# Performance work log

Hardware: AMD Instinct MI355X
Metric: run time of the kernel (lower is better)

Reference implementation:

```python
import jax, jax.numpy as jnp
import numpy as np

BETA_F = 1000.0
BETA_B = 1.0
CLAMP = 12.0
B, C, H, W = 4, 1, 1024, 1024
N_NODES = 262144  # nodes per max-tree


def soft_mask(logits):
    # forward sigmoid with beta_f gain and +-12 clamp (clamp_logits=True)
    return jax.nn.sigmoid(jnp.clip(BETA_F * logits, -CLAMP, CLAMP))


def tree_filter(sigma, levels, parent):
    """Differentiable connected filtering on one max-tree.
    Node value = level(root) + sum over root->node path of sigma_j*(level_j - level_parent_j),
    computed with pointer-doubling ancestor sums (log N gather passes).
    sigma, levels: (N,), parent: (N,) int32 with parent[0]==0 (root).
    """
    N = sigma.shape[0]
    delta = levels - levels[parent]          # per-node gray-level increment
    c = (sigma * delta).at[0].set(levels[0])  # root contributes its level
    # sentinel node N with contribution 0 and self-pointer, terminates chains
    acc = jnp.concatenate([c, jnp.zeros((1,), c.dtype)])
    ptr = jnp.concatenate([parent.at[0].set(N), jnp.full((1,), N, parent.dtype)])
    steps = int(np.ceil(np.log2(N))) + 1
    for _ in range(steps):
        acc, ptr = acc + acc[ptr], ptr[ptr]
    return acc[:N]


def setup_inputs() -> dict:
    rng = np.random.default_rng(0)
    T = B * C  # one tree per (b, c) image
    idx = np.arange(N_NODES)
    # topologically ordered random tree: parent[i] in [0, i), parent[0] = 0
    parent = np.floor(rng.random((T, N_NODES)) * idx).astype(np.int32)
    # monotone increasing gray levels: ancestor-sum of positive increments
    inc = (rng.random((T, N_NODES)) + 0.1).astype(np.float32)
    acc = np.concatenate([inc, np.zeros((T, 1), np.float32)], 1)
    ptr = np.concatenate([parent, np.full((T, 1), N_NODES, np.int64)], 1)
    ptr[:, 0] = N_NODES
    for _ in range(int(np.ceil(np.log2(N_NODES))) + 1):
        acc = acc + np.take_along_axis(acc, ptr, 1)
        ptr = np.take_along_axis(ptr, ptr, 1)
    levels = acc[:, :N_NODES]
    attr_norm = rng.random((T, N_NODES)).astype(np.float32)  # minmax01-normalized attribute
    pixel_to_node = rng.integers(0, N_NODES, (T, H * W)).astype(np.int32)
    x = rng.standard_normal((B, C, H, W)).astype(np.float32)
    return {
        "x": jnp.asarray(x),
        "attr_norm": jnp.asarray(attr_norm),
        "levels": jnp.asarray(levels),
        "thr": jnp.full((1,), 0.5, jnp.float32),  # torch init.constant_(p, 0.5)
        "parent": jnp.asarray(parent),
        "pixel_to_node": jnp.asarray(pixel_to_node),
    }


def reference(x, attr_norm, levels, thr, parent, pixel_to_node):
    # logits = attr_scaled - threshold_norm, per node, per tree
    sigma = soft_mask(attr_norm - thr.reshape(()))          # (T, N)
    v = jax.vmap(tree_filter)(sigma, levels, parent)         # (T, N) filtered node values
    y = jnp.take_along_axis(v, pixel_to_node, axis=1)        # node -> pixel gather
    return y.reshape(B, C, H, W)  # top_hat=False, num_groups=1 -> out_channels=C
```

## Files before the change

### kernel.cpp

```cpp
#include <hip/hip_runtime.h>

#define NT 4
#define NN 262144
#define NMASK (NN - 1)
#define HW 1048576
#define KPRE 16384

#define SWIZ(b, tree, chunk)                \
    int tree  = ((b) & 7) >> 1;             \
    int chunk = (((b) >> 3) << 1) | ((b) & 1);

__global__ __launch_bounds__(256) void k_build(const float* __restrict__ attr,
                                               const float* __restrict__ levels,
                                               const float* __restrict__ thr,
                                               const int* __restrict__ parent,
                                               int2* __restrict__ cmb) {
    SWIZ(blockIdx.x, tree, chunk)
    int n = chunk * 256 + threadIdx.x;
    int i = (tree << 18) + n;
    int p = parent[i] & NMASK;
    float lv = levels[i];
    float lp = levels[(tree << 18) | p];
    float z = 1000.0f * (attr[i] - thr[0]);
    z = fminf(fmaxf(z, -12.0f), 12.0f);
    float s = 1.0f / (1.0f + __expf(-z));
    float c = s * (lv - lp);
    if (n == 0) { c = lv; p = 0; }
    cmb[i] = make_int2(p, __float_as_int(c));
}

__global__ __launch_bounds__(256) void k_prefix(const int2* __restrict__ cmb,
                                                float* __restrict__ v) {
    SWIZ(blockIdx.x, tree, chunk)
    int node = chunk * 256 + threadIdx.x;
    const int2* ctree = cmb + (tree << 18);
    float acc = 0.0f;
    int cur = node;
    bool alive = true;
    for (int it = 0; it < 64 && __any(alive); ++it) {
        if (alive) {
            int2 rec = ctree[cur];
            acc += __int_as_float(rec.y);
            if (cur == 0) alive = false;
            else cur = rec.x;
        }
    }
    v[(tree << 18) + node] = acc;
}

__global__ __launch_bounds__(256) void k_walk(const int2* __restrict__ cmb,
                                              float* __restrict__ v) {
    SWIZ(blockIdx.x, tree, chunk)
    int base = KPRE + chunk * 1024;
    const int2*  ctree = cmb + (tree << 18);
    const float* vtree = v + (tree << 18);

    int   cur[4];
    float acc[4];
    int alive = 0xF;
#pragma unroll
    for (int k = 0; k < 4; ++k) {
        cur[k] = base + threadIdx.x + k * 256;
        acc[k] = 0.0f;
    }
    for (int it = 0; it < 64 && __any(alive); ++it) {
#pragma unroll
        for (int k = 0; k < 4; ++k) {
            if (alive & (1 << k)) {
                int2 rec = ctree[cur[k]];
                acc[k] += __int_as_float(rec.y);
                int nxt = rec.x;
                if (nxt < KPRE) {
                    acc[k] += vtree[nxt];
                    alive &= ~(1 << k);
                } else {
                    cur[k] = nxt;
                }
            }
        }
    }
#pragma unroll
    for (int k = 0; k < 4; ++k)
        v[(tree << 18) + base + threadIdx.x + k * 256] = acc[k];
}

__global__ __launch_bounds__(256) void k_pix(const float* __restrict__ v,
                                             const int* __restrict__ p2n,
                                             float* __restrict__ y) {
    SWIZ(blockIdx.x, tree, chunk)
    int i = (tree << 18) + chunk * 256 + threadIdx.x;
    int4 idx = ((const int4*)p2n)[i];
    const float* vt = v + (tree << 18);
    float4 o;
    o.x = vt[idx.x & NMASK];
    o.y = vt[idx.y & NMASK];
    o.z = vt[idx.z & NMASK];
    o.w = vt[idx.w & NMASK];
    ((float4*)y)[i] = o;
}

extern "C" void kernel_launch(void* const* d_in, const int* in_sizes, int n_in,
                              void* d_out, int out_size, void* d_ws, size_t ws_size,
                              hipStream_t stream) {
    const float* attr   = (const float*)d_in[1];
    const float* levels = (const float*)d_in[2];
    const float* thr    = (const float*)d_in[3];
    const int*   parent = (const int*)d_in[4];
    const int*   p2n    = (const int*)d_in[5];
    float*       y      = (float*)d_out;

    int2*  cmb = (int2*)d_ws;
    float* v   = (float*)((char*)d_ws + (size_t)NT * NN * sizeof(int2));

    k_build <<<NT * NN / 256, 256, 0, stream>>>(attr, levels, thr, parent, cmb);
    k_prefix<<<NT * KPRE / 256, 256, 0, stream>>>(cmb, v);
    k_walk  <<<NT * (NN - KPRE) / 1024, 256, 0, stream>>>(cmb, v);
    k_pix   <<<NT * HW / 4 / 256, 256, 0, stream>>>(v, p2n, y);
}
```

Baseline: 135.1 us.

## Rebalance two-phase tree walk split point and vectorize build with nontemporal loads

Moves the boundary between the direct root-walk phase and the shortcut phase from 16K to 64K nodes, and makes the second phase walk one node per thread instead of four. The build kernel now handles four nodes per thread with vector and nontemporal loads and stores, and the pixel gather uses nontemporal index loads and output stores. The larger first phase does longer full-depth walks, but it lets second-phase chains end sooner at a precomputed ancestor. The trade-off is more work in phase A against less in phase B.

Result: faster. 131.1 us, median of 2 (-2.9%).

```diff
diff --git a/kernel.cpp b/kernel.cpp
--- a/kernel.cpp
+++ b/kernel.cpp
@@ -4,99 +4,105 @@
 #define NN 262144
 #define NMASK (NN - 1)
 #define HW 1048576
-#define KPRE 16384
+#define KB 65536
 
-#define SWIZ(b, tree, chunk)                \
-    int tree  = ((b) & 7) >> 1;             \
+typedef int   vi4 __attribute__((ext_vector_type(4)));
+typedef float vf4 __attribute__((ext_vector_type(4)));
+
+#define SWIZ(b, tree, chunk)                      \
+    int tree  = ((b) & 7) >> 1;                   \
     int chunk = (((b) >> 3) << 1) | ((b) & 1);
 
-__global__ __launch_bounds__(256) void k_build(const float* __restrict__ attr,
-                                               const float* __restrict__ levels,
-                                               const float* __restrict__ thr,
-                                               const int* __restrict__ parent,
-                                               int2* __restrict__ cmb) {
+__global__ __launch_bounds__(256, 4) void k_build(
+        const float* __restrict__ attr,
+        const float* __restrict__ levels,
+        const float* __restrict__ thr,
+        const int*   __restrict__ parent,
+        int2*        __restrict__ cmb) {
     SWIZ(blockIdx.x, tree, chunk)
-    int n = chunk * 256 + threadIdx.x;
-    int i = (tree << 18) + n;
-    int p = parent[i] & NMASK;
-    float lv = levels[i];
-    float lp = levels[(tree << 18) | p];
-    float z = 1000.0f * (attr[i] - thr[0]);
-    z = fminf(fmaxf(z, -12.0f), 12.0f);
-    float s = 1.0f / (1.0f + __expf(-z));
-    float c = s * (lv - lp);
-    if (n == 0) { c = lv; p = 0; }
-    cmb[i] = make_int2(p, __float_as_int(c));
+    int tb = tree << 18;
+    int n0 = (chunk * 256 + threadIdx.x) * 4;
+    int i0 = tb + n0;
+    vi4 p4 = __builtin_nontemporal_load((const vi4*)(parent + i0));
+    vf4 a4 = __builtin_nontemporal_load((const vf4*)(attr + i0));
+    vf4 l4 = *(const vf4*)(levels + i0);
+    float th = thr[0];
+    int2 out[4];
+#pragma unroll
+    for (int k = 0; k < 4; ++k) {
+        int p = p4[k] & NMASK;
+        float lp = levels[tb | p];
+        float z = 1000.0f * (a4[k] - th);
+        z = fminf(fmaxf(z, -12.0f), 12.0f);
+        float s = 1.0f / (1.0f + __expf(-z));
+        float c = s * (l4[k] - lp);
+        if (n0 + k == 0) { c = l4[k]; p = 0; }
+        out[k] = make_int2(p, __float_as_int(c));
+    }
+    vi4 o0 = { out[0].x, out[0].y, out[1].x, out[1].y };
+    vi4 o1 = { out[2].x, out[2].y, out[3].x, out[3].y };
+    *(vi4*)(cmb + i0)     = o0;
+    *(vi4*)(cmb + i0 + 2) = o1;
 }
 
-__global__ __launch_bounds__(256) void k_prefix(const int2* __restrict__ cmb,
-                                                float* __restrict__ v) {
+__global__ __launch_bounds__(256, 4) void k_walkA(
+        const int2* __restrict__ cmb,
+        float*      __restrict__ v) {
     SWIZ(blockIdx.x, tree, chunk)
+    int tb   = tree << 18;
     int node = chunk * 256 + threadIdx.x;
-    const int2* ctree = cmb + (tree << 18);
+    const int2* ct = cmb + tb;
     float acc = 0.0f;
     int cur = node;
     bool alive = true;
     for (int it = 0; it < 64 && __any(alive); ++it) {
         if (alive) {
-            int2 rec = ctree[cur];
-            acc += __int_as_float(rec.y);
+            int2 r = ct[cur];
+            acc += __int_as_float(r.y);
             if (cur == 0) alive = false;
-            else cur = rec.x;
+            else cur = r.x;
         }
     }
-    v[(tree << 18) + node] = acc;
+    v[tb + node] = acc;
 }
 
-__global__ __launch_bounds__(256) void k_walk(const int2* __restrict__ cmb,
-                                              float* __restrict__ v) {
+__global__ __launch_bounds__(256, 4) void k_walkB(
+        const int2* __restrict__ cmb,
+        float*      __restrict__ v) {
     SWIZ(blockIdx.x, tree, chunk)
-    int base = KPRE + chunk * 1024;
-    const int2*  ctree = cmb + (tree << 18);
-    const float* vtree = v + (tree << 18);
-
-    int   cur[4];
-    float acc[4];
-    int alive = 0xF;
-#pragma unroll
-    for (int k = 0; k < 4; ++k) {
-        cur[k] = base + threadIdx.x + k * 256;
-        acc[k] = 0.0f;
-    }
+    int tb   = tree << 18;
+    int node = KB + chunk * 256 + threadIdx.x;
+    const int2*  ct = cmb + tb;
+    const float* vt = v + tb;
+    float acc = 0.0f;
+    int cur = node;
+    bool alive = true;
     for (int it = 0; it < 64 && __any(alive); ++it) {
-#pragma unroll
-        for (int k = 0; k < 4; ++k) {
-            if (alive & (1 << k)) {
-                int2 rec = ctree[cur[k]];
-                acc[k] += __int_as_float(rec.y);
-                int nxt = rec.x;
-                if (nxt < KPRE) {
-                    acc[k] += vtree[nxt];
-                    alive &= ~(1 << k);
-                } else {
-                    cur[k] = nxt;
-                }
-            }
+        if (alive) {
+            int2 r = ct[cur];
+            acc += __int_as_float(r.y);
+            int nxt = r.x;
+            if (nxt < KB) { acc += vt[nxt]; alive = false; }
+            else cur = nxt;
         }
     }
-#pragma unroll
-    for (int k = 0; k < 4; ++k)
-        v[(tree << 18) + base + threadIdx.x + k * 256] = acc[k];
+    v[tb + node] = acc;
 }
 
-__global__ __launch_bounds__(256) void k_pix(const float* __restrict__ v,
-                                             const int* __restrict__ p2n,
-                                             float* __restrict__ y) {
+__global__ __launch_bounds__(256, 4) void k_pix(
+        const float* __restrict__ v,
+        const int*   __restrict__ p2n,
+        float*       __restrict__ y) {
     SWIZ(blockIdx.x, tree, chunk)
     int i = (tree << 18) + chunk * 256 + threadIdx.x;
-    int4 idx = ((const int4*)p2n)[i];
+    vi4 idx = __builtin_nontemporal_load((const vi4*)p2n + i);
     const float* vt = v + (tree << 18);
-    float4 o;
+    vf4 o;
     o.x = vt[idx.x & NMASK];
     o.y = vt[idx.y & NMASK];
     o.z = vt[idx.z & NMASK];
     o.w = vt[idx.w & NMASK];
-    ((float4*)y)[i] = o;
+    __builtin_nontemporal_store(o, (vf4*)y + i);
 }
 
 extern "C" void kernel_launch(void* const* d_in, const int* in_sizes, int n_in,
@@ -112,8 +118,8 @@
     int2*  cmb = (int2*)d_ws;
     float* v   = (float*)((char*)d_ws + (size_t)NT * NN * sizeof(int2));
 
-    k_build <<<NT * NN / 256, 256, 0, stream>>>(attr, levels, thr, parent, cmb);
-    k_prefix<<<NT * KPRE / 256, 256, 0, stream>>>(cmb, v);
-    k_walk  <<<NT * (NN - KPRE) / 1024, 256, 0, stream>>>(cmb, v);
-    k_pix   <<<NT * HW / 4 / 256, 256, 0, stream>>>(v, p2n, y);
+    k_build<<<NT * NN / 4 / 256, 256, 0, stream>>>(attr, levels, thr, parent, cmb);
+    k_walkA<<<NT * KB / 256, 256, 0, stream>>>(cmb, v);
+    k_walkB<<<NT * (NN - KB) / 256, 256, 0, stream>>>(cmb, v);
+    k_pix  <<<NT * HW / 4 / 256, 256, 0, stream>>>(v, p2n, y);
 }
```
